# Kernel tuning notes

Measured on AMD Instinct MI355X. Metric: run time of the kernel, lower is better.

The kernel has to match this reference:

```python
import jax, jax.numpy as jnp
import numpy as np

B, T, E, H = 8, 1024, 1024, 16
D = E // H  # head_dim = 64
MAX_OFFSET = 0.5


def setup_inputs() -> dict:
    key = jax.random.key(0)
    ks = jax.random.split(key, 12)
    s = 0.02
    return {
        "query": jax.random.normal(ks[0], (B, T, E), jnp.float32),
        "key_": jax.random.normal(ks[1], (B, T, E), jnp.float32),
        "value": jax.random.normal(ks[2], (B, T, E), jnp.float32),
        "Wq": jax.random.normal(ks[3], (E, E), jnp.float32) * s,
        "bq": jnp.zeros((E,), jnp.float32),
        "Wk": jax.random.normal(ks[4], (E, E), jnp.float32) * s,
        "bk": jnp.zeros((E,), jnp.float32),
        "Wv": jax.random.normal(ks[5], (E, E), jnp.float32) * s,
        "bv": jnp.zeros((E,), jnp.float32),
        "Wo": jax.random.normal(ks[6], (E, E), jnp.float32) * s,
        "bo": jnp.zeros((E,), jnp.float32),
        "bias_table": jax.random.normal(ks[7], (2 * T - 1, H), jnp.float32) * s,
        "offset": jax.random.normal(ks[8], (1,), jnp.float32) * 0.1,
    }


def _temporal_bias(bias_table, offset):
    # relative position index: [T, T] in [0, 2T-2]
    coords = jnp.arange(T)
    rel = (coords[:, None] - coords[None, :]) + (T - 1)
    bounded = jnp.tanh(offset) * MAX_OFFSET  # scalar (shape (1,))
    adj = jnp.clip(rel.astype(jnp.float32) + bounded, 0.0, 2.0 * T - 2.0)
    lo = jnp.floor(adj).astype(jnp.int32)
    hi = jnp.ceil(adj).astype(jnp.int32)
    w = adj - lo.astype(jnp.float32)  # [T, T]
    lo_val = bias_table[lo]  # [T, T, H]
    hi_val = bias_table[hi]  # [T, T, H]
    bias = lo_val * (1.0 - w[..., None]) + hi_val * w[..., None]
    # -> [1, H, T, T]
    return jnp.transpose(bias, (2, 0, 1))[None]


def reference(query, key_, value, Wq, bq, Wk, bk, Wv, bv, Wo, bo, bias_table, offset):
    scale = D ** -0.5
    # torch Linear: x @ W.T + b
    q = (jnp.einsum('bte,fe->btf', query, Wq) + bq).reshape(B, T, H, D).transpose(0, 2, 1, 3)
    k = (jnp.einsum('bte,fe->btf', key_, Wk) + bk).reshape(B, T, H, D).transpose(0, 2, 1, 3)
    v = (jnp.einsum('bte,fe->btf', value, Wv) + bv).reshape(B, T, H, D).transpose(0, 2, 1, 3)
    scores = jnp.einsum('bhqd,bhkd->bhqk', q, k) * scale  # [B, H, T, T]
    scores = scores + _temporal_bias(bias_table, offset)
    attn = jax.nn.softmax(scores, axis=-1)
    out = jnp.einsum('bhqk,bhkd->bhqd', attn, v)  # [B, H, T, D]
    out = out.transpose(0, 2, 1, 3).reshape(B, T, E)
    return jnp.einsum('bte,fe->btf', out, Wo) + bo
```

## Files before the change

kernel.cpp:

```cpp
#include <hip/hip_runtime.h>
#include <hip/hip_bf16.h>
#include <stdint.h>

#define B_ 8
#define T_ 1024
#define E_ 1024
#define H_ 16
#define D_ 64
#define NREL 2047

using bf16 = __hip_bfloat16;
typedef __attribute__((ext_vector_type(8))) short bhalf8;
typedef __attribute__((ext_vector_type(4))) float f32x4;

typedef __attribute__((address_space(3))) uint32_t lds32_t;
typedef const __attribute__((address_space(1))) uint32_t glb32_t;
__device__ __forceinline__ void gld_lds16(const void* g, void* l) {
  __builtin_amdgcn_global_load_lds((glb32_t*)g, (lds32_t*)l, 16, 0, 0);
}

__device__ __forceinline__ bhalf8 cvt8(const float4 a, const float4 b) {
  bf16 t[8];
  t[0] = __float2bfloat16(a.x); t[1] = __float2bfloat16(a.y);
  t[2] = __float2bfloat16(a.z); t[3] = __float2bfloat16(a.w);
  t[4] = __float2bfloat16(b.x); t[5] = __float2bfloat16(b.y);
  t[6] = __float2bfloat16(b.z); t[7] = __float2bfloat16(b.w);
  return *(const bhalf8*)t;
}

__global__ __launch_bounds__(256) void cvt_w4b(const float* __restrict__ Wq,
                                               const float* __restrict__ Wk,
                                               const float* __restrict__ Wv,
                                               const float* __restrict__ Wo,
                                               bf16* __restrict__ d,
                                               const float* __restrict__ table,
                                               const float* __restrict__ offset,
                                               float* __restrict__ db) {
  const int z = blockIdx.y;
  if (z == 4) {
    const int idx = blockIdx.x * 256 + threadIdx.x;
    if (idx >= NREL * H_) return;
    const int r = idx >> 4;
    const int h = idx & 15;
    const float bounded = tanhf(offset[0]) * 0.5f;
    float adj = (float)r + bounded;
    adj = fminf(fmaxf(adj, 0.f), 2046.f);
    const int lo = (int)floorf(adj);
    const int hi = (int)ceilf(adj);
    const float wgt = adj - (float)lo;
    const float v = table[lo * H_ + h] * (1.f - wgt) + table[hi * H_ + h] * wgt;
    db[h * NREL + r] = v * 1.4426950408889634f;
    return;
  }
  const float* s = (z == 0) ? Wq : (z == 1) ? Wk : (z == 2) ? Wv : Wo;
  const int i = (blockIdx.x * 256 + threadIdx.x) * 8;
  const float4 a = *(const float4*)(s + i);
  const float4 b = *(const float4*)(s + i + 4);
  *(bhalf8*)(d + (size_t)z * E_ * E_ + i) = cvt8(a, b);
}

__global__ __launch_bounds__(256, 3) void gemm_qkv(const float* __restrict__ Xq,
                                                   const float* __restrict__ Xk,
                                                   const float* __restrict__ Xv,
                                                   const bf16* __restrict__ Wc,
                                                   const float* __restrict__ bqp,
                                                   const float* __restrict__ bkp,
                                                   const float* __restrict__ bvp,
                                                   bf16* __restrict__ dst) {
  __shared__ float AsF[2 * 128 * 32];
  __shared__ bf16 Bs[2 * 128 * 32];
  const int tid = threadIdx.x;
  const int lane = tid & 63;
  const int w = tid >> 6;
  const int quad = lane >> 4;
  const int l15 = lane & 15;
  const int m0 = blockIdx.x * 128;
  const int n0 = blockIdx.y * 128;
  const int z = blockIdx.z;
  const float* A = (z == 0) ? Xq : ((z == 1) ? Xk : Xv);
  const float* bias = (z == 0) ? bqp : ((z == 1) ? bkp : bvp);
  const bf16* W = Wc + (size_t)z * E_ * E_;
  bf16* out = dst + (size_t)z * B_ * T_ * D_ * H_;
  const int wm = (w >> 1) * 64;
  const int wn = (w & 1) * 64;

  const f32x4 zero4 = {0.f, 0.f, 0.f, 0.f};
  f32x4 acc[4][4];
#pragma unroll
  for (int i = 0; i < 4; ++i)
#pragma unroll
    for (int j = 0; j < 4; ++j) acc[i][j] = zero4;

  const int g = tid;
  const int arow = g >> 3;
  const int acol = (((g & 7) ^ ((g >> 3) & 7)) << 2);
  const float* Ag = A + (size_t)(m0 + arow) * E_ + acol;
  float* AsDst = AsF + g * 4;
  const int srowW = w * 32 + (lane >> 2);
  const int scolW = (lane & 3) * 8;
  const bf16* Wg = W + (size_t)(n0 + srowW) * E_ + scolW;
  bf16* BsDst = Bs + w * 1024 + lane * 8;

#pragma unroll
  for (int c = 0; c < 4; ++c)
    gld_lds16(Ag + (size_t)c * 32 * E_, AsDst + c * 1024);
  gld_lds16(Wg, BsDst);
  gld_lds16(Wg + (size_t)16 * E_, BsDst + 512);
  __syncthreads();

  for (int kt = 0; kt < 32; ++kt) {
    const int curA = (kt & 1) * 4096;
    const int curB = (kt & 1) * 4096;
    bhalf8 af[4], bfr[4];
#pragma unroll
    for (int mt = 0; mt < 4; ++mt) {
      const int row = wm + mt * 16 + l15;
      const int cb = (quad * 32) ^ ((row & 7) << 4);
      const char* rp = (const char*)(AsF + curA + row * 32);
      const float4 lo = *(const float4*)(rp + cb);
      const float4 hi = *(const float4*)(rp + (cb ^ 16));
      af[mt] = cvt8(lo, hi);
    }
#pragma unroll
    for (int nt = 0; nt < 4; ++nt)
      bfr[nt] = *(const bhalf8*)(Bs + curB + (wn + nt * 16 + l15) * 32 + quad * 8);
    if (kt < 31) {
      const int nxtA = 4096 - curA;
      const int nxtB = 4096 - curB;
      const int kc = (kt + 1) * 32;
#pragma unroll
      for (int c = 0; c < 4; ++c)
        gld_lds16(Ag + (size_t)c * 32 * E_ + kc, AsDst + nxtA + c * 1024);
      gld_lds16(Wg + kc, BsDst + nxtB);
      gld_lds16(Wg + (size_t)16 * E_ + kc, BsDst + nxtB + 512);
    }
#pragma unroll
    for (int mt = 0; mt < 4; ++mt)
#pragma unroll
      for (int nt = 0; nt < 4; ++nt)
        acc[mt][nt] = __builtin_amdgcn_mfma_f32_16x16x32_bf16(af[mt], bfr[nt], acc[mt][nt], 0, 0, 0);
    __syncthreads();
  }

#pragma unroll
  for (int mt = 0; mt < 4; ++mt) {
#pragma unroll
    for (int nt = 0; nt < 4; ++nt) {
      const int n = n0 + wn + nt * 16 + l15;
      const float bv = bias[n];
#pragma unroll
      for (int r = 0; r < 4; ++r) {
        const int m = m0 + wm + mt * 16 + quad * 4 + r;
        const float v = acc[mt][nt][r] + bv;
        const int bb = m >> 10, tq = m & 1023, hh = n >> 6, d = n & 63;
        out[(((size_t)bb * H_ + hh) * T_ + tq) * D_ + d] = __float2bfloat16(v);
      }
    }
  }
}

template <int SCATTER, int F32OUT>
__global__ __launch_bounds__(256, 4) void gemm_bt(const bf16* __restrict__ A,
                                                  const bf16* __restrict__ W,
                                                  const float* __restrict__ bias,
                                                  void* __restrict__ dst_) {
  __shared__ bf16 As[2 * 64 * 32];
  __shared__ bf16 Bs[2 * 128 * 32];
  const int tid = threadIdx.x;
  const int lane = tid & 63;
  const int w = tid >> 6;
  const int quad = lane >> 4;
  const int l15 = lane & 15;
  const int m0 = blockIdx.x * 64;
  const int n0 = blockIdx.y * 128;
  const int wm = (w >> 1) * 32;
  const int wn = (w & 1) * 64;

  const f32x4 zero4 = {0.f, 0.f, 0.f, 0.f};
  f32x4 acc[2][4];
#pragma unroll
  for (int i = 0; i < 2; ++i)
#pragma unroll
    for (int j = 0; j < 4; ++j) acc[i][j] = zero4;

  const int scol = (lane & 3) * 8;
  const int srowA = w * 16 + (lane >> 2);
  const bf16* Ag = A + (size_t)(m0 + srowA) * E_ + scol;
  const int sidxA = w * 512 + lane * 8;
  const int srowB = w * 32 + (lane >> 2);
  const bf16* Wg = W + (size_t)(n0 + srowB) * E_ + scol;
  const int sidxB = w * 1024 + lane * 8;

  gld_lds16(Ag, As + sidxA);
  gld_lds16(Wg, Bs + sidxB);
  gld_lds16(Wg + (size_t)16 * E_, Bs + sidxB + 512);
  __syncthreads();

  for (int kt = 0; kt < 32; ++kt) {
    const int curA = (kt & 1) * 2048;
    const int curB = (kt & 1) * 4096;
    bhalf8 af[2], bfr[4];
#pragma unroll
    for (int mt = 0; mt < 2; ++mt)
      af[mt] = *(const bhalf8*)(As + curA + (wm + mt * 16 + l15) * 32 + quad * 8);
#pragma unroll
    for (int nt = 0; nt < 4; ++nt)
      bfr[nt] = *(const bhalf8*)(Bs + curB + (wn + nt * 16 + l15) * 32 + quad * 8);
    if (kt < 31) {
      const int nxtA = 2048 - curA;
      const int nxtB = 4096 - curB;
      const int kc = (kt + 1) * 32;
      gld_lds16(Ag + kc, As + nxtA + sidxA);
      gld_lds16(Wg + kc, Bs + nxtB + sidxB);
      gld_lds16(Wg + (size_t)16 * E_ + kc, Bs + nxtB + sidxB + 512);
    }
#pragma unroll
    for (int mt = 0; mt < 2; ++mt)
#pragma unroll
      for (int nt = 0; nt < 4; ++nt)
        acc[mt][nt] = __builtin_amdgcn_mfma_f32_16x16x32_bf16(af[mt], bfr[nt], acc[mt][nt], 0, 0, 0);
    __syncthreads();
  }

#pragma unroll
  for (int mt = 0; mt < 2; ++mt) {
#pragma unroll
    for (int nt = 0; nt < 4; ++nt) {
      const int n = n0 + wn + nt * 16 + l15;
      const float bv = bias[n];
#pragma unroll
      for (int r = 0; r < 4; ++r) {
        const int m = m0 + wm + mt * 16 + quad * 4 + r;
        const float v = acc[mt][nt][r] + bv;
        if (SCATTER) {
          const int bb = m >> 10, t = m & 1023, hh = n >> 6, d = n & 63;
          ((bf16*)dst_)[(((size_t)bb * H_ + hh) * T_ + t) * D_ + d] = __float2bfloat16(v);
        } else if (F32OUT) {
          ((float*)dst_)[(size_t)m * E_ + n] = v;
        } else {
          ((bf16*)dst_)[(size_t)m * E_ + n] = __float2bfloat16(v);
        }
      }
    }
  }
}

__device__ __forceinline__ int ps_off(int row, int colbyte) {
  return row * 128 + (colbyte ^ ((row & 7) << 4));
}

__global__ __launch_bounds__(256, 4) void attn_kernel(const bf16* __restrict__ Q,
                                                      const bf16* __restrict__ K,
                                                      const bf16* __restrict__ V,
                                                      const float* __restrict__ db,
                                                      bf16* __restrict__ xout) {
  const int tid = threadIdx.x;
  const int lane = tid & 63;
  const int w = tid >> 6;
  const int quad = lane >> 4;
  const int l15 = lane & 15;
  const int bh = blockIdx.x;
  const int h = bh & 15;
  const int b = bh >> 4;
  const int q0 = blockIdx.y * 128;

  __shared__ bf16 Vt[64][72];
  __shared__ __align__(16) bf16 Ps[4][32 * 64];
  __shared__ float dbs[1152];

  const size_t base = (size_t)bh * T_ * D_;
  const bf16* Qp = Q + base;
  const bf16* Kp = K + base;
  const bf16* Vp = V + base;
  const float* dbh = db + h * NREL;

  for (int t = tid; t < 1151; t += 256) dbs[t] = dbh[q0 + t];

  const int qw = q0 + w * 32;
  bhalf8 aq[2][2];
#pragma unroll
  for (int mt = 0; mt < 2; ++mt)
#pragma unroll
    for (int ks = 0; ks < 2; ++ks)
      aq[mt][ks] = *(const bhalf8*)(Qp + (size_t)(qw + mt * 16 + l15) * D_ + ks * 32 + quad * 8);

  const f32x4 zero4 = {0.f, 0.f, 0.f, 0.f};
  f32x4 o[2][4];
#pragma unroll
  for (int mt = 0; mt < 2; ++mt)
#pragma unroll
    for (int nt = 0; nt < 4; ++nt) o[mt][nt] = zero4;
  float mrow[2] = {-1e30f, -1e30f};
  float lrow[2] = {0.f, 0.f};

  const int vrow0 = tid >> 3;
  const int vc8 = (tid & 7) * 8;
  bhalf8 vreg[2];
  vreg[0] = *(const bhalf8*)(Vp + (size_t)vrow0 * D_ + vc8);
  vreg[1] = *(const bhalf8*)(Vp + (size_t)(vrow0 + 32) * D_ + vc8);

  char* const psw = (char*)&Ps[w][0];

  for (int it = 0; it < 16; ++it) {
    const int kb = it * 64;
    bhalf8 bk[4][2];
#pragma unroll
    for (int nt = 0; nt < 4; ++nt) {
      const bf16* kr = Kp + (size_t)(kb + nt * 16 + l15) * D_ + quad * 8;
      bk[nt][0] = *(const bhalf8*)kr;
      bk[nt][1] = *(const bhalf8*)(kr + 32);
    }

    __syncthreads();
#pragma unroll
    for (int s = 0; s < 2; ++s) {
      const int row = vrow0 + s * 32;
      const bf16* vp = (const bf16*)&vreg[s];
      const int kvp = (row + vc8) & 63;
#pragma unroll
      for (int j = 0; j < 8; ++j) Vt[vc8 + j][kvp] = vp[j];
    }
    __syncthreads();
    if (it < 15) {
      const int kb2 = kb + 64;
      vreg[0] = *(const bhalf8*)(Vp + (size_t)(kb2 + vrow0) * D_ + vc8);
      vreg[1] = *(const bhalf8*)(Vp + (size_t)(kb2 + vrow0 + 32) * D_ + vc8);
    }

    f32x4 s4[2][4];
    __builtin_amdgcn_s_setprio(1);
#pragma unroll
    for (int nt = 0; nt < 4; ++nt) {
#pragma unroll
      for (int mt = 0; mt < 2; ++mt) {
        f32x4 a = zero4;
        a = __builtin_amdgcn_mfma_f32_16x16x32_bf16(bk[nt][0], aq[mt][0], a, 0, 0, 0);
        a = __builtin_amdgcn_mfma_f32_16x16x32_bf16(bk[nt][1], aq[mt][1], a, 0, 0, 0);
        s4[mt][nt] = a;
      }
    }
    __builtin_amdgcn_s_setprio(0);

#pragma unroll
    for (int mt = 0; mt < 2; ++mt) {
      const int ib = w * 32 + mt * 16 + l15 + 1023 - kb;
      float mnt[4];
#pragma unroll
      for (int nt = 0; nt < 4; ++nt) {
#pragma unroll
        for (int r = 0; r < 4; ++r) {
          const float sv = s4[mt][nt][r] * 0.18033688011112042f + dbs[ib - nt * 16 - quad * 4 - r];
          s4[mt][nt][r] = sv;
        }
        mnt[nt] = fmaxf(fmaxf(s4[mt][nt][0], s4[mt][nt][1]),
                        fmaxf(s4[mt][nt][2], s4[mt][nt][3]));
      }
      float tmx = fmaxf(fmaxf(mnt[0], mnt[1]), fmaxf(mnt[2], mnt[3]));
      tmx = fmaxf(tmx, __shfl_xor(tmx, 16, 64));
      tmx = fmaxf(tmx, __shfl_xor(tmx, 32, 64));
      if (!__all(tmx - mrow[mt] <= 11.0f)) {
        const float mnew = fmaxf(mrow[mt], tmx);
        const float alpha = __builtin_amdgcn_exp2f(mrow[mt] - mnew);
        mrow[mt] = mnew;
        lrow[mt] *= alpha;
#pragma unroll
        for (int nt = 0; nt < 4; ++nt) o[mt][nt] *= alpha;
      }
      const float mcur = mrow[mt];
      float psum[4];
#pragma unroll
      for (int nt = 0; nt < 4; ++nt) {
        float p0 = __builtin_amdgcn_exp2f(s4[mt][nt][0] - mcur);
        float p1 = __builtin_amdgcn_exp2f(s4[mt][nt][1] - mcur);
        float p2 = __builtin_amdgcn_exp2f(s4[mt][nt][2] - mcur);
        float p3 = __builtin_amdgcn_exp2f(s4[mt][nt][3] - mcur);
        s4[mt][nt][0] = p0; s4[mt][nt][1] = p1;
        s4[mt][nt][2] = p2; s4[mt][nt][3] = p3;
        psum[nt] = (p0 + p1) + (p2 + p3);
      }
      float sum = (psum[0] + psum[1]) + (psum[2] + psum[3]);
      sum += __shfl_xor(sum, 16, 64);
      sum += __shfl_xor(sum, 32, 64);
      lrow[mt] += sum;

#pragma unroll
      for (int nt = 0; nt < 4; ++nt) {
        alignas(8) bf16 t4[4];
#pragma unroll
        for (int r = 0; r < 4; ++r) t4[r] = __float2bfloat16(s4[mt][nt][r]);
        *(uint2*)(psw + ps_off(mt * 16 + l15, nt * 32 + quad * 8)) = *(const uint2*)t4;
      }
    }

    bhalf8 pb[2][2];
#pragma unroll
    for (int mt = 0; mt < 2; ++mt)
#pragma unroll
      for (int ks = 0; ks < 2; ++ks)
        pb[mt][ks] = *(const bhalf8*)(psw + ps_off(mt * 16 + l15, ks * 64 + quad * 16));
    const int rot = (l15 >> 3);
    __builtin_amdgcn_s_setprio(1);
#pragma unroll
    for (int nt = 0; nt < 4; ++nt) {
      const int drow = nt * 16 + l15;
#pragma unroll
      for (int ks = 0; ks < 2; ++ks) {
        const int gp = (4 * ks + quad + 2 * nt + rot) & 7;
        const bhalf8 vb = *(const bhalf8*)&Vt[drow][gp * 8];
#pragma unroll
        for (int mt = 0; mt < 2; ++mt)
          o[mt][nt] = __builtin_amdgcn_mfma_f32_16x16x32_bf16(vb, pb[mt][ks], o[mt][nt], 0, 0, 0);
      }
    }
    __builtin_amdgcn_s_setprio(0);
  }

#pragma unroll
  for (int mt = 0; mt < 2; ++mt) {
    const float inv = 1.f / lrow[mt];
#pragma unroll
    for (int nt = 0; nt < 4; ++nt) {
      alignas(8) bf16 t4[4];
#pragma unroll
      for (int r = 0; r < 4; ++r) t4[r] = __float2bfloat16(o[mt][nt][r] * inv);
      *(uint2*)(psw + ps_off(mt * 16 + l15, nt * 32 + quad * 8)) = *(const uint2*)t4;
    }
  }
#pragma unroll
  for (int t = 0; t < 4; ++t) {
    const int idx = t * 64 + lane;
    const int row = idx >> 3;
    const int c = idx & 7;
    const bhalf8 val = *(const bhalf8*)(psw + ps_off(row, c * 16));
    *(bhalf8*)&xout[((size_t)b * T_ + qw + row) * E_ + h * D_ + c * 8] = val;
  }
}

extern "C" void kernel_launch(void* const* d_in, const int* in_sizes, int n_in,
                              void* d_out, int out_size, void* d_ws, size_t ws_size,
                              hipStream_t stream) {
  const float* query = (const float*)d_in[0];
  const float* key_  = (const float*)d_in[1];
  const float* value = (const float*)d_in[2];
  const float* Wq = (const float*)d_in[3];
  const float* bq = (const float*)d_in[4];
  const float* Wk = (const float*)d_in[5];
  const float* bk = (const float*)d_in[6];
  const float* Wv = (const float*)d_in[7];
  const float* bv = (const float*)d_in[8];
  const float* Wo = (const float*)d_in[9];
  const float* bo = (const float*)d_in[10];
  const float* table = (const float*)d_in[11];
  const float* offset = (const float*)d_in[12];
  float* out = (float*)d_out;

  char* ws = (char*)d_ws;
  const size_t ME = (size_t)B_ * T_ * E_;
  const size_t EE = (size_t)E_ * E_;
  float* db = (float*)ws;
  bf16* wc  = (bf16*)(ws + 131072);
  bf16* qb  = wc + 4 * EE;
  bf16* kb  = qb + ME;
  bf16* vb2 = kb + ME;
  bf16* x2  = vb2 + ME;

  dim3 bb(256, 1, 1);
  const int gEE = (int)(EE / 8 / 256);

  cvt_w4b<<<dim3(gEE, 5), bb, 0, stream>>>(Wq, Wk, Wv, Wo, wc, table, offset, db);

  gemm_qkv<<<dim3(64, 8, 3), bb, 0, stream>>>(query, key_, value, wc, bq, bk, bv, qb);

  attn_kernel<<<dim3(128, 8, 1), bb, 0, stream>>>(qb, kb, vb2, db, x2);

  gemm_bt<0, 1><<<dim3(128, 8, 1), bb, 0, stream>>>(x2, wc + 3 * EE, bo, out);
}
```

Measured before the change: 352.2 us.

## Enlarge output GEMM tile to 128x128 and stage 128 keys of V per barrier

```diff
diff --git a/kernel.cpp b/kernel.cpp
--- a/kernel.cpp
+++ b/kernel.cpp
@@ -160,62 +160,59 @@
 }
 
 template <int SCATTER, int F32OUT>
-__global__ __launch_bounds__(256, 4) void gemm_bt(const bf16* __restrict__ A,
-                                                  const bf16* __restrict__ W,
-                                                  const float* __restrict__ bias,
-                                                  void* __restrict__ dst_) {
-  __shared__ bf16 As[2 * 64 * 32];
+__global__ __launch_bounds__(256) void gemm_bt(const bf16* __restrict__ A,
+                                               const bf16* __restrict__ W,
+                                               const float* __restrict__ bias,
+                                               void* __restrict__ dst_) {
+  __shared__ bf16 As[2 * 128 * 32];
   __shared__ bf16 Bs[2 * 128 * 32];
   const int tid = threadIdx.x;
   const int lane = tid & 63;
   const int w = tid >> 6;
   const int quad = lane >> 4;
   const int l15 = lane & 15;
-  const int m0 = blockIdx.x * 64;
+  const int m0 = blockIdx.x * 128;
   const int n0 = blockIdx.y * 128;
-  const int wm = (w >> 1) * 32;
+  const int wm = (w >> 1) * 64;
   const int wn = (w & 1) * 64;
 
   const f32x4 zero4 = {0.f, 0.f, 0.f, 0.f};
-  f32x4 acc[2][4];
-#pragma unroll
-  for (int i = 0; i < 2; ++i)
+  f32x4 acc[4][4];
+#pragma unroll
+  for (int i = 0; i < 4; ++i)
 #pragma unroll
     for (int j = 0; j < 4; ++j) acc[i][j] = zero4;
 
+  const int srow0 = w * 32 + (lane >> 2);
   const int scol = (lane & 3) * 8;
-  const int srowA = w * 16 + (lane >> 2);
-  const bf16* Ag = A + (size_t)(m0 + srowA) * E_ + scol;
-  const int sidxA = w * 512 + lane * 8;
-  const int srowB = w * 32 + (lane >> 2);
-  const bf16* Wg = W + (size_t)(n0 + srowB) * E_ + scol;
-  const int sidxB = w * 1024 + lane * 8;
-
-  gld_lds16(Ag, As + sidxA);
-  gld_lds16(Wg, Bs + sidxB);
-  gld_lds16(Wg + (size_t)16 * E_, Bs + sidxB + 512);
+  const bf16* Ag = A + (size_t)(m0 + srow0) * E_ + scol;
+  const bf16* Wg = W + (size_t)(n0 + srow0) * E_ + scol;
+  const int sidx = w * 1024 + lane * 8;
+
+  gld_lds16(Ag, As + sidx);
+  gld_lds16(Ag + (size_t)16 * E_, As + sidx + 512);
+  gld_lds16(Wg, Bs + sidx);
+  gld_lds16(Wg + (size_t)16 * E_, Bs + sidx + 512);
   __syncthreads();
 
   for (int kt = 0; kt < 32; ++kt) {
-    const int curA = (kt & 1) * 2048;
-    const int curB = (kt & 1) * 4096;
-    bhalf8 af[2], bfr[4];
-#pragma unroll
-    for (int mt = 0; mt < 2; ++mt)
-      af[mt] = *(const bhalf8*)(As + curA + (wm + mt * 16 + l15) * 32 + quad * 8);
-#pragma unroll
-    for (int nt = 0; nt < 4; ++nt)
-      bfr[nt] = *(const bhalf8*)(Bs + curB + (wn + nt * 16 + l15) * 32 + quad * 8);
+    const int cur = (kt & 1) * 4096;
+    bhalf8 af[4], bfr[4];
+#pragma unroll
+    for (int t = 0; t < 4; ++t) {
+      af[t] = *(const bhalf8*)(As + cur + (wm + t * 16 + l15) * 32 + quad * 8);
+      bfr[t] = *(const bhalf8*)(Bs + cur + (wn + t * 16 + l15) * 32 + quad * 8);
+    }
     if (kt < 31) {
-      const int nxtA = 2048 - curA;
-      const int nxtB = 4096 - curB;
+      const int nxt = 4096 - cur;
       const int kc = (kt + 1) * 32;
-      gld_lds16(Ag + kc, As + nxtA + sidxA);
-      gld_lds16(Wg + kc, Bs + nxtB + sidxB);
-      gld_lds16(Wg + (size_t)16 * E_ + kc, Bs + nxtB + sidxB + 512);
-    }
-#pragma unroll
-    for (int mt = 0; mt < 2; ++mt)
+      gld_lds16(Ag + kc, As + nxt + sidx);
+      gld_lds16(Ag + (size_t)16 * E_ + kc, As + nxt + sidx + 512);
+      gld_lds16(Wg + kc, Bs + nxt + sidx);
+      gld_lds16(Wg + (size_t)16 * E_ + kc, Bs + nxt + sidx + 512);
+    }
+#pragma unroll
+    for (int mt = 0; mt < 4; ++mt)
 #pragma unroll
       for (int nt = 0; nt < 4; ++nt)
         acc[mt][nt] = __builtin_amdgcn_mfma_f32_16x16x32_bf16(af[mt], bfr[nt], acc[mt][nt], 0, 0, 0);
@@ -223,7 +220,7 @@
   }
 
 #pragma unroll
-  for (int mt = 0; mt < 2; ++mt) {
+  for (int mt = 0; mt < 4; ++mt) {
 #pragma unroll
     for (int nt = 0; nt < 4; ++nt) {
       const int n = n0 + wn + nt * 16 + l15;
@@ -259,12 +256,13 @@
   const int w = tid >> 6;
   const int quad = lane >> 4;
   const int l15 = lane & 15;
-  const int bh = blockIdx.x;
+  const int n = blockIdx.x;
+  const int bh = n & 127;
   const int h = bh & 15;
   const int b = bh >> 4;
-  const int q0 = blockIdx.y * 128;
-
-  __shared__ bf16 Vt[64][72];
+  const int q0 = (n >> 7) * 128;
+
+  __shared__ bf16 Vt[2][64][72];
   __shared__ __align__(16) bf16 Ps[4][32 * 64];
   __shared__ float dbs[1152];
 
@@ -295,124 +293,141 @@
 
   const int vrow0 = tid >> 3;
   const int vc8 = (tid & 7) * 8;
-  bhalf8 vreg[2];
+  bhalf8 vreg[4];
   vreg[0] = *(const bhalf8*)(Vp + (size_t)vrow0 * D_ + vc8);
   vreg[1] = *(const bhalf8*)(Vp + (size_t)(vrow0 + 32) * D_ + vc8);
+  vreg[2] = *(const bhalf8*)(Vp + (size_t)(64 + vrow0) * D_ + vc8);
+  vreg[3] = *(const bhalf8*)(Vp + (size_t)(64 + vrow0 + 32) * D_ + vc8);
 
   char* const psw = (char*)&Ps[w][0];
-
-  for (int it = 0; it < 16; ++it) {
-    const int kb = it * 64;
+  const int rot = (l15 >> 3);
+
+  for (int pt = 0; pt < 8; ++pt) {
+    const int kb0 = pt * 128;
     bhalf8 bk[4][2];
 #pragma unroll
     for (int nt = 0; nt < 4; ++nt) {
-      const bf16* kr = Kp + (size_t)(kb + nt * 16 + l15) * D_ + quad * 8;
+      const bf16* kr = Kp + (size_t)(kb0 + nt * 16 + l15) * D_ + quad * 8;
       bk[nt][0] = *(const bhalf8*)kr;
       bk[nt][1] = *(const bhalf8*)(kr + 32);
     }
 
     __syncthreads();
 #pragma unroll
-    for (int s = 0; s < 2; ++s) {
-      const int row = vrow0 + s * 32;
+    for (int s = 0; s < 4; ++s) {
+      const int row = vrow0 + (s & 1) * 32;
       const bf16* vp = (const bf16*)&vreg[s];
       const int kvp = (row + vc8) & 63;
 #pragma unroll
-      for (int j = 0; j < 8; ++j) Vt[vc8 + j][kvp] = vp[j];
+      for (int j = 0; j < 8; ++j) Vt[s >> 1][vc8 + j][kvp] = vp[j];
     }
     __syncthreads();
-    if (it < 15) {
-      const int kb2 = kb + 64;
+    if (pt < 7) {
+      const int kb2 = kb0 + 128;
       vreg[0] = *(const bhalf8*)(Vp + (size_t)(kb2 + vrow0) * D_ + vc8);
       vreg[1] = *(const bhalf8*)(Vp + (size_t)(kb2 + vrow0 + 32) * D_ + vc8);
-    }
-
-    f32x4 s4[2][4];
-    __builtin_amdgcn_s_setprio(1);
-#pragma unroll
-    for (int nt = 0; nt < 4; ++nt) {
+      vreg[2] = *(const bhalf8*)(Vp + (size_t)(kb2 + 64 + vrow0) * D_ + vc8);
+      vreg[3] = *(const bhalf8*)(Vp + (size_t)(kb2 + 64 + vrow0 + 32) * D_ + vc8);
+    }
+
+#pragma unroll
+    for (int half = 0; half < 2; ++half) {
+      const int kb = kb0 + half * 64;
+      if (half == 1) {
+#pragma unroll
+        for (int nt = 0; nt < 4; ++nt) {
+          const bf16* kr = Kp + (size_t)(kb + nt * 16 + l15) * D_ + quad * 8;
+          bk[nt][0] = *(const bhalf8*)kr;
+          bk[nt][1] = *(const bhalf8*)(kr + 32);
+        }
+      }
+
+      f32x4 s4[2][4];
+      __builtin_amdgcn_s_setprio(1);
+#pragma unroll
+      for (int nt = 0; nt < 4; ++nt) {
+#pragma unroll
+        for (int mt = 0; mt < 2; ++mt) {
+          f32x4 a = zero4;
+          a = __builtin_amdgcn_mfma_f32_16x16x32_bf16(bk[nt][0], aq[mt][0], a, 0, 0, 0);
+          a = __builtin_amdgcn_mfma_f32_16x16x32_bf16(bk[nt][1], aq[mt][1], a, 0, 0, 0);
+          s4[mt][nt] = a;
+        }
+      }
+      __builtin_amdgcn_s_setprio(0);
+
 #pragma unroll
       for (int mt = 0; mt < 2; ++mt) {
-        f32x4 a = zero4;
-        a = __builtin_amdgcn_mfma_f32_16x16x32_bf16(bk[nt][0], aq[mt][0], a, 0, 0, 0);
-        a = __builtin_amdgcn_mfma_f32_16x16x32_bf16(bk[nt][1], aq[mt][1], a, 0, 0, 0);
-        s4[mt][nt] = a;
-      }
-    }
-    __builtin_amdgcn_s_setprio(0);
-
-#pragma unroll
-    for (int mt = 0; mt < 2; ++mt) {
-      const int ib = w * 32 + mt * 16 + l15 + 1023 - kb;
-      float mnt[4];
+        const int ib = w * 32 + mt * 16 + l15 + 1023 - kb;
+        float mnt[4];
+#pragma unroll
+        for (int nt = 0; nt < 4; ++nt) {
+#pragma unroll
+          for (int r = 0; r < 4; ++r) {
+            const float sv = s4[mt][nt][r] * 0.18033688011112042f + dbs[ib - nt * 16 - quad * 4 - r];
+            s4[mt][nt][r] = sv;
+          }
+          mnt[nt] = fmaxf(fmaxf(s4[mt][nt][0], s4[mt][nt][1]),
+                          fmaxf(s4[mt][nt][2], s4[mt][nt][3]));
+        }
+        float tmx = fmaxf(fmaxf(mnt[0], mnt[1]), fmaxf(mnt[2], mnt[3]));
+        tmx = fmaxf(tmx, __shfl_xor(tmx, 16, 64));
+        tmx = fmaxf(tmx, __shfl_xor(tmx, 32, 64));
+        if (!__all(tmx - mrow[mt] <= 11.0f)) {
+          const float mnew = fmaxf(mrow[mt], tmx);
+          const float alpha = __builtin_amdgcn_exp2f(mrow[mt] - mnew);
+          mrow[mt] = mnew;
+          lrow[mt] *= alpha;
+#pragma unroll
+          for (int nt = 0; nt < 4; ++nt) o[mt][nt] *= alpha;
+        }
+        const float mcur = mrow[mt];
+        float psum[4];
+#pragma unroll
+        for (int nt = 0; nt < 4; ++nt) {
+          float p0 = __builtin_amdgcn_exp2f(s4[mt][nt][0] - mcur);
+          float p1 = __builtin_amdgcn_exp2f(s4[mt][nt][1] - mcur);
+          float p2 = __builtin_amdgcn_exp2f(s4[mt][nt][2] - mcur);
+          float p3 = __builtin_amdgcn_exp2f(s4[mt][nt][3] - mcur);
+          s4[mt][nt][0] = p0; s4[mt][nt][1] = p1;
+          s4[mt][nt][2] = p2; s4[mt][nt][3] = p3;
+          psum[nt] = (p0 + p1) + (p2 + p3);
+        }
+        float sum = (psum[0] + psum[1]) + (psum[2] + psum[3]);
+        sum += __shfl_xor(sum, 16, 64);
+        sum += __shfl_xor(sum, 32, 64);
+        lrow[mt] += sum;
+
+#pragma unroll
+        for (int nt = 0; nt < 4; ++nt) {
+          alignas(8) bf16 t4[4];
+#pragma unroll
+          for (int r = 0; r < 4; ++r) t4[r] = __float2bfloat16(s4[mt][nt][r]);
+          *(uint2*)(psw + ps_off(mt * 16 + l15, nt * 32 + quad * 8)) = *(const uint2*)t4;
+        }
+      }
+
+      bhalf8 pb[2][2];
+#pragma unroll
+      for (int mt = 0; mt < 2; ++mt)
+#pragma unroll
+        for (int ks = 0; ks < 2; ++ks)
+          pb[mt][ks] = *(const bhalf8*)(psw + ps_off(mt * 16 + l15, ks * 64 + quad * 16));
+      __builtin_amdgcn_s_setprio(1);
 #pragma unroll
       for (int nt = 0; nt < 4; ++nt) {
-#pragma unroll
-        for (int r = 0; r < 4; ++r) {
-          const float sv = s4[mt][nt][r] * 0.18033688011112042f + dbs[ib - nt * 16 - quad * 4 - r];
-          s4[mt][nt][r] = sv;
-        }
-        mnt[nt] = fmaxf(fmaxf(s4[mt][nt][0], s4[mt][nt][1]),
-                        fmaxf(s4[mt][nt][2], s4[mt][nt][3]));
-      }
-      float tmx = fmaxf(fmaxf(mnt[0], mnt[1]), fmaxf(mnt[2], mnt[3]));
-      tmx = fmaxf(tmx, __shfl_xor(tmx, 16, 64));
-      tmx = fmaxf(tmx, __shfl_xor(tmx, 32, 64));
-      if (!__all(tmx - mrow[mt] <= 11.0f)) {
-        const float mnew = fmaxf(mrow[mt], tmx);
-        const float alpha = __builtin_amdgcn_exp2f(mrow[mt] - mnew);
-        mrow[mt] = mnew;
-        lrow[mt] *= alpha;
-#pragma unroll
-        for (int nt = 0; nt < 4; ++nt) o[mt][nt] *= alpha;
-      }
-      const float mcur = mrow[mt];
-      float psum[4];
-#pragma unroll
-      for (int nt = 0; nt < 4; ++nt) {
-        float p0 = __builtin_amdgcn_exp2f(s4[mt][nt][0] - mcur);
-        float p1 = __builtin_amdgcn_exp2f(s4[mt][nt][1] - mcur);
-        float p2 = __builtin_amdgcn_exp2f(s4[mt][nt][2] - mcur);
-        float p3 = __builtin_amdgcn_exp2f(s4[mt][nt][3] - mcur);
-        s4[mt][nt][0] = p0; s4[mt][nt][1] = p1;
-        s4[mt][nt][2] = p2; s4[mt][nt][3] = p3;
-        psum[nt] = (p0 + p1) + (p2 + p3);
-      }
-      float sum = (psum[0] + psum[1]) + (psum[2] + psum[3]);
-      sum += __shfl_xor(sum, 16, 64);
-      sum += __shfl_xor(sum, 32, 64);
-      lrow[mt] += sum;
-
-#pragma unroll
-      for (int nt = 0; nt < 4; ++nt) {
-        alignas(8) bf16 t4[4];
-#pragma unroll
-        for (int r = 0; r < 4; ++r) t4[r] = __float2bfloat16(s4[mt][nt][r]);
-        *(uint2*)(psw + ps_off(mt * 16 + l15, nt * 32 + quad * 8)) = *(const uint2*)t4;
-      }
-    }
-
-    bhalf8 pb[2][2];
-#pragma unroll
-    for (int mt = 0; mt < 2; ++mt)
-#pragma unroll
-      for (int ks = 0; ks < 2; ++ks)
-        pb[mt][ks] = *(const bhalf8*)(psw + ps_off(mt * 16 + l15, ks * 64 + quad * 16));
-    const int rot = (l15 >> 3);
-    __builtin_amdgcn_s_setprio(1);
-#pragma unroll
-    for (int nt = 0; nt < 4; ++nt) {
-      const int drow = nt * 16 + l15;
-#pragma unroll
-      for (int ks = 0; ks < 2; ++ks) {
-        const int gp = (4 * ks + quad + 2 * nt + rot) & 7;
-        const bhalf8 vb = *(const bhalf8*)&Vt[drow][gp * 8];
-#pragma unroll
-        for (int mt = 0; mt < 2; ++mt)
-          o[mt][nt] = __builtin_amdgcn_mfma_f32_16x16x32_bf16(vb, pb[mt][ks], o[mt][nt], 0, 0, 0);
-      }
-    }
-    __builtin_amdgcn_s_setprio(0);
+        const int drow = nt * 16 + l15;
+#pragma unroll
+        for (int ks = 0; ks < 2; ++ks) {
+          const int gp = (4 * ks + quad + 2 * nt + rot) & 7;
+          const bhalf8 vb = *(const bhalf8*)&Vt[half][drow][gp * 8];
+#pragma unroll
+          for (int mt = 0; mt < 2; ++mt)
+            o[mt][nt] = __builtin_amdgcn_mfma_f32_16x16x32_bf16(vb, pb[mt][ks], o[mt][nt], 0, 0, 0);
+        }
+      }
+      __builtin_amdgcn_s_setprio(0);
+    }
   }
 
 #pragma unroll
@@ -471,7 +486,7 @@
 
   gemm_qkv<<<dim3(64, 8, 3), bb, 0, stream>>>(query, key_, value, wc, bq, bk, bv, qb);
 
-  attn_kernel<<<dim3(128, 8, 1), bb, 0, stream>>>(qb, kb, vb2, db, x2);
-
-  gemm_bt<0, 1><<<dim3(128, 8, 1), bb, 0, stream>>>(x2, wc + 3 * EE, bo, out);
-}
+  attn_kernel<<<dim3(1024), bb, 0, stream>>>(qb, kb, vb2, db, x2);
+
+  gemm_bt<0, 1><<<dim3(64, 8, 1), bb, 0, stream>>>(x2, wc + 3 * EE, bo, out);
+}
```

New measurement: 358.3 us. No clear change (+1.7%).
